# Optimization experiments

Hardware: AMD Instinct MI355X
Metric: run time of the kernel (lower is better)

The kernel has to match this reference:

```python
import jax, jax.numpy as jnp
import numpy as np

T, B, NIN = 256, 256, 512
NH, NEMB = 512, 256


def setup_inputs() -> dict:
    key = jax.random.key(0)
    ks = jax.random.split(key, 11)
    s = 0.02  # small init to keep tanh/sigmoid in active range
    return {
        "feats": jax.random.normal(ks[0], (T, B, NIN), jnp.float32),
        "h": jax.random.normal(ks[1], (B, NH), jnp.float32),
        "cur_embed": jax.random.normal(ks[2], (B, NEMB), jnp.float32),
        # i2h: Linear(nIn, nHidden, bias=False)
        "w_i2h": jax.random.normal(ks[3], (NH, NIN), jnp.float32) * s,
        # h2h: Linear(nHidden, nHidden) with bias
        "w_h2h": jax.random.normal(ks[4], (NH, NH), jnp.float32) * s,
        "b_h2h": jax.random.normal(ks[5], (NH,), jnp.float32) * s,
        # score: Linear(nHidden, 1, bias=False)
        "w_score": jax.random.normal(ks[6], (NH,), jnp.float32) * s,
        # GRUCell(nIn + num_embeddings, nHidden); gate order r, z, n
        "w_ih": jax.random.normal(ks[7], (3 * NH, NIN + NEMB), jnp.float32) * s,
        "w_hh": jax.random.normal(ks[8], (3 * NH, NH), jnp.float32) * s,
        "b_ih": jax.random.normal(ks[9], (3 * NH,), jnp.float32) * s,
        "b_hh": jax.random.normal(ks[10], (3 * NH,), jnp.float32) * s,
    }


def reference(feats, h, cur_embed, w_i2h, w_h2h, b_h2h, w_score,
              w_ih, w_hh, b_ih, b_hh):
    # MORAN branch, test=True (FractionalPickup is skipped at eval time).
    # feats: [T, B, nIn], h: [B, nHidden], cur_embed: [B, nEmb]
    feats_ = jnp.einsum('tbc,hc->tbh', feats, w_i2h)          # i2h, [T,B,H]
    h_ = h @ w_h2h.T + b_h2h                                   # h2h, [B,H]
    emit = jnp.einsum('tbh,h->tb', jnp.tanh(feats_ + h_[None]), w_score)
    alpha = jax.nn.softmax(emit, axis=0)                       # softmax over T
    context = jnp.einsum('tb,tbc->bc', alpha, feats)           # [B,nIn]
    x = jnp.concatenate([context, cur_embed], axis=1)          # [B,nIn+nEmb]
    # GRUCell
    gi = x @ w_ih.T + b_ih                                     # [B,3H]
    gh = h @ w_hh.T + b_hh                                     # [B,3H]
    gi_r, gi_z, gi_n = jnp.split(gi, 3, axis=1)
    gh_r, gh_z, gh_n = jnp.split(gh, 3, axis=1)
    r = jax.nn.sigmoid(gi_r + gh_r)
    z = jax.nn.sigmoid(gi_z + gh_z)
    n = jnp.tanh(gi_n + r * gh_n)
    nh = (1.0 - z) * n + z * h
    return nh, alpha
```

## Files before the change

### kernel.cpp

```cpp
#include <hip/hip_runtime.h>

typedef __bf16 bf16;
typedef __bf16 bf16x4 __attribute__((ext_vector_type(4)));
typedef __bf16 bf16x8 __attribute__((ext_vector_type(8)));
typedef float  f32x4  __attribute__((ext_vector_type(4)));

#define T_DIM 256
#define B_DIM 256
#define NIN   512
#define NH    512
#define NEMB  256
#define NX    768
#define NG    1536
#define MTOT  65536

__device__ __forceinline__ float fast_tanh(float x) {
    float e = __expf(2.0f * x);
    return 1.0f - 2.0f * __builtin_amdgcn_rcpf(e + 1.0f);
}
__device__ __forceinline__ float fast_sigmoid(float x) {
    return __builtin_amdgcn_rcpf(1.0f + __expf(-x));
}

__device__ __forceinline__ void gload_lds16(const bf16* g, bf16* l) {
    __builtin_amdgcn_global_load_lds(
        (const __attribute__((address_space(1))) void*)g,
        (__attribute__((address_space(3))) void*)l, 16, 0, 0);
}

__device__ __forceinline__ int csw(int row) { return (row >> 1) & 3; }

__global__ __launch_bounds__(256) void cvt_weights(
    const float* __restrict__ a0, const float* __restrict__ a1,
    const float* __restrict__ a2, const float* __restrict__ a3,
    const float* __restrict__ a4,
    bf16* __restrict__ b0, bf16* __restrict__ b1, bf16* __restrict__ b2,
    bf16* __restrict__ b3, bf16* __restrict__ b4) {
    const int N0 = 65536, N1 = 131072, N2 = 425984, N3 = 622592, N4 = 655360;
    for (int i = blockIdx.x * 256 + threadIdx.x; i < N4; i += gridDim.x * 256) {
        const float* s; bf16* d; int j;
        if (i < N0)      { s = a0; d = b0; j = i; }
        else if (i < N1) { s = a1; d = b1; j = i - N0; }
        else if (i < N2) { s = a2; d = b2; j = i - N1; }
        else if (i < N3) { s = a3; d = b3; j = i - N2; }
        else             { s = a4; d = b4; j = i - N3; }
        float4 v = reinterpret_cast<const float4*>(s)[j];
        bf16x4 o = { (bf16)v.x, (bf16)v.y, (bf16)v.z, (bf16)v.w };
        reinterpret_cast<bf16x4*>(d)[j] = o;
    }
}

__global__ __launch_bounds__(256) void gemm_bias(
    const bf16* __restrict__ A, const bf16* __restrict__ B,
    const float* __restrict__ bias, float* __restrict__ C,
    int M, int N, int K) {
    __shared__ bf16 At[64][40];
    __shared__ bf16 Bt[64][40];
    const int tid = threadIdx.x;
    const int m0 = blockIdx.y * 64, n0 = blockIdx.x * 64;
    const int wid = tid >> 6, lane = tid & 63, hi = lane >> 4, lo = lane & 15;
    const int srow = tid >> 2, sseg = tid & 3;
    f32x4 acc[4] = {};

    for (int kk = 0; kk < K; kk += 32) {
        bf16x8 av = *reinterpret_cast<const bf16x8*>(A + (size_t)(m0 + srow) * K + kk + sseg * 8);
        bf16x8 bv = *reinterpret_cast<const bf16x8*>(B + (size_t)(n0 + srow) * K + kk + sseg * 8);
        __syncthreads();
        *reinterpret_cast<bf16x8*>(&At[srow][sseg * 8]) = av;
        *reinterpret_cast<bf16x8*>(&Bt[srow][sseg * 8]) = bv;
        __syncthreads();
        bf16x8 a = *reinterpret_cast<const bf16x8*>(&At[wid * 16 + lo][hi * 8]);
#pragma unroll
        for (int nt = 0; nt < 4; ++nt) {
            bf16x8 b = *reinterpret_cast<const bf16x8*>(&Bt[nt * 16 + lo][hi * 8]);
            acc[nt] = __builtin_amdgcn_mfma_f32_16x16x32_bf16(a, b, acc[nt], 0, 0, 0);
        }
    }
#pragma unroll
    for (int nt = 0; nt < 4; ++nt) {
        int n = n0 + nt * 16 + lo;
        float bv = bias[n];
#pragma unroll
        for (int r = 0; r < 4; ++r) {
            int m = m0 + wid * 16 + hi * 4 + r;
            C[(size_t)m * N + n] = acc[nt][r] + bv;
        }
    }
}

__global__ __launch_bounds__(256, 3) void emit_kernel(
    const float* __restrict__ feats, const bf16* __restrict__ Wb,
    const float* __restrict__ hbuf, const float* __restrict__ wscore,
    float* __restrict__ emit_part) {
    __shared__ bf16 At[128 * 32];
    __shared__ bf16 Bt[128 * 32];
    __shared__ float ew[4][64];
    const int tid = threadIdx.x;
    const int tile = (blockIdx.x & 7) * 256 + (blockIdx.x >> 3);
    const int nb = tile & 3, mb = tile >> 2;
    const int m0 = mb * 128, n0g = nb * 128;
    const int wid = tid >> 6, lane = tid & 63, hi = lane >> 4, lo = lane & 15;
    const int wr = wid >> 1, wc = wid & 1;

    const int ar0 = tid >> 2, ac0 = tid & 3;
    const int ar1 = 64 + ar0, ac1 = ac0;
    const float* as0 = feats + (size_t)(m0 + ar0) * NIN + ac0 * 8;
    const float* as1 = feats + (size_t)(m0 + ar1) * NIN + ac1 * 8;
    bf16* aw0 = At + ar0 * 32 + ((ac0 ^ csw(ar0)) * 8);
    bf16* aw1 = At + ar1 * 32 + ((ac1 ^ csw(ar1)) * 8);
    const bf16* bs0 = Wb + (size_t)(n0g + ar0) * NIN + ((ac0 ^ csw(ar0)) * 8);
    const bf16* bs1 = Wb + (size_t)(n0g + ar1) * NIN + ((ac1 ^ csw(ar1)) * 8);
    bf16* bd0 = Bt + wid * 512;
    bf16* bd1 = Bt + 2048 + wid * 512;

    float4 f00 = *reinterpret_cast<const float4*>(as0);
    float4 f01 = *reinterpret_cast<const float4*>(as0 + 4);
    float4 f10 = *reinterpret_cast<const float4*>(as1);
    float4 f11 = *reinterpret_cast<const float4*>(as1 + 4);

    f32x4 acc[4][4] = {};
#pragma unroll
    for (int kk = 0; kk < 16; ++kk) {
        if (kk > 0) __syncthreads();
        bf16x8 o0 = { (bf16)f00.x, (bf16)f00.y, (bf16)f00.z, (bf16)f00.w,
                      (bf16)f01.x, (bf16)f01.y, (bf16)f01.z, (bf16)f01.w };
        bf16x8 o1 = { (bf16)f10.x, (bf16)f10.y, (bf16)f10.z, (bf16)f10.w,
                      (bf16)f11.x, (bf16)f11.y, (bf16)f11.z, (bf16)f11.w };
        *reinterpret_cast<bf16x8*>(aw0) = o0;
        *reinterpret_cast<bf16x8*>(aw1) = o1;
        gload_lds16(bs0 + kk * 32, bd0);
        gload_lds16(bs1 + kk * 32, bd1);
        __syncthreads();
        if (kk < 15) {
            f00 = *reinterpret_cast<const float4*>(as0 + (kk + 1) * 32);
            f01 = *reinterpret_cast<const float4*>(as0 + (kk + 1) * 32 + 4);
            f10 = *reinterpret_cast<const float4*>(as1 + (kk + 1) * 32);
            f11 = *reinterpret_cast<const float4*>(as1 + (kk + 1) * 32 + 4);
        }
        bf16x8 a[4], b[4];
#pragma unroll
        for (int st = 0; st < 4; ++st) {
            int row = wr * 64 + st * 16 + lo;
            a[st] = *reinterpret_cast<const bf16x8*>(
                At + row * 32 + ((hi ^ csw(row)) * 8));
        }
#pragma unroll
        for (int nt = 0; nt < 4; ++nt) {
            int col = wc * 64 + nt * 16 + lo;
            b[nt] = *reinterpret_cast<const bf16x8*>(
                Bt + col * 32 + ((hi ^ csw(col)) * 8));
        }
#pragma unroll
        for (int nt = 0; nt < 4; ++nt)
#pragma unroll
            for (int st = 0; st < 4; ++st)
                acc[nt][st] = __builtin_amdgcn_mfma_f32_16x16x32_bf16(
                    a[st], b[nt], acc[nt][st], 0, 0, 0);
    }

    float ep[4][4] = {};
    const int bbase = m0 & (B_DIM - 1);
#pragma unroll
    for (int nt = 0; nt < 4; ++nt) {
        int n = n0g + wc * 64 + nt * 16 + lo;
        float wsn = wscore[n];
#pragma unroll
        for (int st = 0; st < 4; ++st) {
#pragma unroll
            for (int r = 0; r < 4; ++r) {
                int b = bbase + wr * 64 + st * 16 + hi * 4 + r;
                float x = acc[nt][st][r] + hbuf[(size_t)b * NH + n];
                ep[st][r] += fast_tanh(x) * wsn;
            }
        }
    }
#pragma unroll
    for (int st = 0; st < 4; ++st)
#pragma unroll
        for (int r = 0; r < 4; ++r)
#pragma unroll
            for (int off = 1; off < 16; off <<= 1)
                ep[st][r] += __shfl_xor(ep[st][r], off, 64);

    if (lo == 0) {
#pragma unroll
        for (int st = 0; st < 4; ++st)
#pragma unroll
            for (int r = 0; r < 4; ++r)
                ew[wid][st * 16 + hi * 4 + r] = ep[st][r];
    }
    __syncthreads();
    if (tid < 128) {
        float s = ew[(tid >> 6) * 2][tid & 63] + ew[(tid >> 6) * 2 + 1][tid & 63];
        emit_part[(size_t)nb * MTOT + m0 + tid] = s;
    }
}

__global__ __launch_bounds__(256) void softmax_t(
    const float* __restrict__ emit_part, float* __restrict__ alpha,
    float* __restrict__ out_alpha) {
    int b = blockIdx.x, t = threadIdx.x;
    int wv = t >> 6, ln = t & 63;
    size_t m = (size_t)t * B_DIM + b;
    float e = emit_part[m] + emit_part[MTOT + m] +
              emit_part[2 * MTOT + m] + emit_part[3 * MTOT + m];
    float mx = e;
#pragma unroll
    for (int off = 32; off; off >>= 1) mx = fmaxf(mx, __shfl_xor(mx, off, 64));
    __shared__ float red[4], red2[4];
    if (ln == 0) red[wv] = mx;
    __syncthreads();
    mx = fmaxf(fmaxf(red[0], red[1]), fmaxf(red[2], red[3]));
    float p = __expf(e - mx);
    float s = p;
#pragma unroll
    for (int off = 32; off; off >>= 1) s += __shfl_xor(s, off, 64);
    if (ln == 0) red2[wv] = s;
    __syncthreads();
    float inv = __builtin_amdgcn_rcpf(red2[0] + red2[1] + red2[2] + red2[3]);
    float a = p * inv;
    alpha[m] = a;
    out_alpha[m] = a;
}

__global__ __launch_bounds__(256) void ctx_kernel(
    const float* __restrict__ feats, const float* __restrict__ alpha,
    const float* __restrict__ emb, bf16* __restrict__ x) {
    int b = blockIdx.x;
    __shared__ float al[T_DIM];
    __shared__ float red[4][512];
    int tid = threadIdx.x;
    al[tid] = alpha[(size_t)tid * B_DIM + b];
    __syncthreads();
    int c8 = tid & 63, tq = tid >> 6;
    float acc[8] = {};
#pragma unroll 4
    for (int t = tq * 64; t < tq * 64 + 64; ++t) {
        const float* src = feats + ((size_t)(t * B_DIM + b)) * NIN + c8 * 8;
        float4 v0 = *reinterpret_cast<const float4*>(src);
        float4 v1 = *reinterpret_cast<const float4*>(src + 4);
        float a = al[t];
        acc[0] += a * v0.x; acc[1] += a * v0.y; acc[2] += a * v0.z; acc[3] += a * v0.w;
        acc[4] += a * v1.x; acc[5] += a * v1.y; acc[6] += a * v1.z; acc[7] += a * v1.w;
    }
#pragma unroll
    for (int j = 0; j < 8; ++j) red[tq][c8 * 8 + j] = acc[j];
    __syncthreads();
#pragma unroll
    for (int k = 0; k < 2; ++k) {
        int c = tid * 2 + k;
        float s = red[0][c] + red[1][c] + red[2][c] + red[3][c];
        x[(size_t)b * NX + c] = (bf16)s;
    }
    x[(size_t)b * NX + NIN + tid] = (bf16)emb[(size_t)b * NEMB + tid];
}

__global__ __launch_bounds__(256) void gru_kernel(
    const float* __restrict__ gi, const float* __restrict__ gh,
    const float* __restrict__ h, float* __restrict__ out) {
    int idx = blockIdx.x * 256 + threadIdx.x;
    int b = idx >> 9, j = idx & 511;
    const float* gib = gi + (size_t)b * NG;
    const float* ghb = gh + (size_t)b * NG;
    float r = fast_sigmoid(gib[j] + ghb[j]);
    float z = fast_sigmoid(gib[NH + j] + ghb[NH + j]);
    float n = fast_tanh(gib[2 * NH + j] + r * ghb[2 * NH + j]);
    out[idx] = (1.0f - z) * n + z * h[idx];
}

extern "C" void kernel_launch(void* const* d_in, const int* in_sizes, int n_in,
                              void* d_out, int out_size, void* d_ws, size_t ws_size,
                              hipStream_t stream) {
    const float* feats = (const float*)d_in[0];
    const float* h     = (const float*)d_in[1];
    const float* emb   = (const float*)d_in[2];
    const float* w_i2h = (const float*)d_in[3];
    const float* w_h2h = (const float*)d_in[4];
    const float* b_h2h = (const float*)d_in[5];
    const float* w_sc  = (const float*)d_in[6];
    const float* w_ih  = (const float*)d_in[7];
    const float* w_hh  = (const float*)d_in[8];
    const float* b_ih  = (const float*)d_in[9];
    const float* b_hh  = (const float*)d_in[10];
    float* out = (float*)d_out;

    char* ws = (char*)d_ws;
    bf16*  w_i2h_b = (bf16*)(ws);
    bf16*  w_h2h_b = (bf16*)(ws + 524288);
    bf16*  w_ih_b  = (bf16*)(ws + 1048576);
    bf16*  w_hh_b  = (bf16*)(ws + 3407872);
    bf16*  h_b     = (bf16*)(ws + 4980736);
    bf16*  x_b     = (bf16*)(ws + 5242880);
    float* hbuf    = (float*)(ws + 5636096);
    float* emit_p  = (float*)(ws + 6160384);
    float* alpha   = (float*)(ws + 7208960);
    float* gi      = (float*)(ws + 7471104);
    float* gh      = (float*)(ws + 9043968);

    cvt_weights<<<1024, 256, 0, stream>>>(w_i2h, w_h2h, w_ih, w_hh, h,
                                          w_i2h_b, w_h2h_b, w_ih_b, w_hh_b, h_b);

    gemm_bias<<<dim3(8, 4), 256, 0, stream>>>(h_b, w_h2h_b, b_h2h, hbuf, 256, NH, NH);
    gemm_bias<<<dim3(24, 4), 256, 0, stream>>>(h_b, w_hh_b, b_hh, gh, 256, NG, NH);

    emit_kernel<<<2048, 256, 0, stream>>>(feats, w_i2h_b, hbuf, w_sc, emit_p);

    softmax_t<<<256, 256, 0, stream>>>(emit_p, alpha, out + 131072);

    ctx_kernel<<<256, 256, 0, stream>>>(feats, alpha, emb, x_b);

    gemm_bias<<<dim3(24, 4), 256, 0, stream>>>(x_b, w_ih_b, b_ih, gi, 256, NG, NX);

    gru_kernel<<<512, 256, 0, stream>>>(gi, gh, h, out);
}
```

Measured before the change: 127.5 us.

## Keep i2h weight fragments in registers and stream feats through double-buffered LDS

The emit kernel is restructured so each wave holds a 32-column slab of the i2h weight as pre-swizzled MFMA fragments in registers for the whole K=512. Each block then streams 512 rows of feats through a double-buffered LDS tile with 32x32x16 MFMAs. The weight conversion kernel now writes w_i2h in that fragment layout, and the grid splits N into two halves instead of four, so softmax sums only two partial emits. This removes the repeated per-tile weight LDS staging and halves the partial-emit traffic. In exchange it uses very high register pressure (32 bf16x8 fragments) and launches only 256 blocks of 512 threads, which may reduce occupancy and latency hiding.

```diff
diff --git a/kernel.cpp b/kernel.cpp
--- a/kernel.cpp
+++ b/kernel.cpp
@@ -4,6 +4,7 @@
 typedef __bf16 bf16x4 __attribute__((ext_vector_type(4)));
 typedef __bf16 bf16x8 __attribute__((ext_vector_type(8)));
 typedef float  f32x4  __attribute__((ext_vector_type(4)));
+typedef float  f32x16 __attribute__((ext_vector_type(16)));
 
 #define T_DIM 256
 #define B_DIM 256
@@ -22,14 +23,6 @@
     return __builtin_amdgcn_rcpf(1.0f + __expf(-x));
 }
 
-__device__ __forceinline__ void gload_lds16(const bf16* g, bf16* l) {
-    __builtin_amdgcn_global_load_lds(
-        (const __attribute__((address_space(1))) void*)g,
-        (__attribute__((address_space(3))) void*)l, 16, 0, 0);
-}
-
-__device__ __forceinline__ int csw(int row) { return (row >> 1) & 3; }
-
 __global__ __launch_bounds__(256) void cvt_weights(
     const float* __restrict__ a0, const float* __restrict__ a1,
     const float* __restrict__ a2, const float* __restrict__ a3,
@@ -38,15 +31,24 @@
     bf16* __restrict__ b3, bf16* __restrict__ b4) {
     const int N0 = 65536, N1 = 131072, N2 = 425984, N3 = 622592, N4 = 655360;
     for (int i = blockIdx.x * 256 + threadIdx.x; i < N4; i += gridDim.x * 256) {
-        const float* s; bf16* d; int j;
-        if (i < N0)      { s = a0; d = b0; j = i; }
+        const float* s; bf16* d; int j; bool img = false;
+        if (i < N0)      { s = a0; d = b0; j = i; img = true; }
         else if (i < N1) { s = a1; d = b1; j = i - N0; }
         else if (i < N2) { s = a2; d = b2; j = i - N1; }
         else if (i < N3) { s = a3; d = b3; j = i - N2; }
         else             { s = a4; d = b4; j = i - N3; }
         float4 v = reinterpret_cast<const float4*>(s)[j];
         bf16x4 o = { (bf16)v.x, (bf16)v.y, (bf16)v.z, (bf16)v.w };
-        reinterpret_cast<bf16x4*>(d)[j] = o;
+        if (img) {
+            int e = j * 4, col = e >> 9, K = e & 511;
+            int g = col >> 5, cl = col & 31;
+            int ks = K >> 4, kh = (K >> 3) & 1, j0 = K & 7;
+            int lane = kh * 32 + cl;
+            int off = (((g * 32 + ks) * 64) + lane) * 8 + j0;
+            *reinterpret_cast<bf16x4*>(d + off) = o;
+        } else {
+            reinterpret_cast<bf16x4*>(d)[j] = o;
+        }
     }
 }
 
@@ -88,111 +90,98 @@
     }
 }
 
-__global__ __launch_bounds__(256, 3) void emit_kernel(
-    const float* __restrict__ feats, const bf16* __restrict__ Wb,
+__global__ __launch_bounds__(512, 2) void emit_kernel(
+    const float* __restrict__ feats, const bf16* __restrict__ Wfrag,
     const float* __restrict__ hbuf, const float* __restrict__ wscore,
     float* __restrict__ emit_part) {
-    __shared__ bf16 At[128 * 32];
-    __shared__ bf16 Bt[128 * 32];
-    __shared__ float ew[4][64];
+    __shared__ bf16 Alds[2][32][516];
+    __shared__ float ew[2][8][32];
     const int tid = threadIdx.x;
-    const int tile = (blockIdx.x & 7) * 256 + (blockIdx.x >> 3);
-    const int nb = tile & 3, mb = tile >> 2;
-    const int m0 = mb * 128, n0g = nb * 128;
-    const int wid = tid >> 6, lane = tid & 63, hi = lane >> 4, lo = lane & 15;
-    const int wr = wid >> 1, wc = wid & 1;
-
-    const int ar0 = tid >> 2, ac0 = tid & 3;
-    const int ar1 = 64 + ar0, ac1 = ac0;
-    const float* as0 = feats + (size_t)(m0 + ar0) * NIN + ac0 * 8;
-    const float* as1 = feats + (size_t)(m0 + ar1) * NIN + ac1 * 8;
-    bf16* aw0 = At + ar0 * 32 + ((ac0 ^ csw(ar0)) * 8);
-    bf16* aw1 = At + ar1 * 32 + ((ac1 ^ csw(ar1)) * 8);
-    const bf16* bs0 = Wb + (size_t)(n0g + ar0) * NIN + ((ac0 ^ csw(ar0)) * 8);
-    const bf16* bs1 = Wb + (size_t)(n0g + ar1) * NIN + ((ac1 ^ csw(ar1)) * 8);
-    bf16* bd0 = Bt + wid * 512;
-    bf16* bd1 = Bt + 2048 + wid * 512;
-
-    float4 f00 = *reinterpret_cast<const float4*>(as0);
-    float4 f01 = *reinterpret_cast<const float4*>(as0 + 4);
-    float4 f10 = *reinterpret_cast<const float4*>(as1);
-    float4 f11 = *reinterpret_cast<const float4*>(as1 + 4);
-
-    f32x4 acc[4][4] = {};
-#pragma unroll
-    for (int kk = 0; kk < 16; ++kk) {
-        if (kk > 0) __syncthreads();
-        bf16x8 o0 = { (bf16)f00.x, (bf16)f00.y, (bf16)f00.z, (bf16)f00.w,
-                      (bf16)f01.x, (bf16)f01.y, (bf16)f01.z, (bf16)f01.w };
-        bf16x8 o1 = { (bf16)f10.x, (bf16)f10.y, (bf16)f10.z, (bf16)f10.w,
-                      (bf16)f11.x, (bf16)f11.y, (bf16)f11.z, (bf16)f11.w };
-        *reinterpret_cast<bf16x8*>(aw0) = o0;
-        *reinterpret_cast<bf16x8*>(aw1) = o1;
-        gload_lds16(bs0 + kk * 32, bd0);
-        gload_lds16(bs1 + kk * 32, bd1);
+    const int wid = tid >> 6, lane = tid & 63;
+    const int half = lane >> 5, l31 = lane & 31;
+    const int slab = blockIdx.x & 1, mb = blockIdx.x >> 1;
+    const int m0 = mb * 512;
+    const int col = slab * 256 + wid * 32 + l31;
+
+    const bf16* wsrc = Wfrag + (size_t)((slab * 8 + wid) * 32) * 512 + lane * 8;
+    bf16x8 bfr[32];
+#pragma unroll
+    for (int ks = 0; ks < 32; ++ks)
+        bfr[ks] = *reinterpret_cast<const bf16x8*>(wsrc + ks * 512);
+
+    const float* asrc = feats + (size_t)m0 * NIN + tid * 4;
+    const int awrow = tid >> 7, awcol = (tid & 127) * 4;
+
+    float4 st[8];
+#pragma unroll
+    for (int j = 0; j < 8; ++j)
+        st[j] = *reinterpret_cast<const float4*>(asrc + j * 2048);
+#pragma unroll
+    for (int j = 0; j < 8; ++j) {
+        bf16x4 o = { (bf16)st[j].x, (bf16)st[j].y, (bf16)st[j].z, (bf16)st[j].w };
+        *reinterpret_cast<bf16x4*>(&Alds[0][awrow + 4 * j][awcol]) = o;
+    }
+    __syncthreads();
+
+    const float wsl = wscore[col];
+
+    for (int it = 0; it < 16; ++it) {
+        const int cur = it & 1;
+        if (it < 15) {
+            const float* an = asrc + (size_t)(it + 1) * 32 * NIN;
+#pragma unroll
+            for (int j = 0; j < 8; ++j)
+                st[j] = *reinterpret_cast<const float4*>(an + j * 2048);
+        }
+
+        f32x16 acc0 = {}, acc1 = {};
+#pragma unroll
+        for (int ks = 0; ks < 32; ks += 2) {
+            const bf16* ap0 = &Alds[cur][l31][ks * 16 + half * 8];
+            bf16x4 p0 = *reinterpret_cast<const bf16x4*>(ap0);
+            bf16x4 p1 = *reinterpret_cast<const bf16x4*>(ap0 + 4);
+            bf16x8 a0 = { p0[0], p0[1], p0[2], p0[3], p1[0], p1[1], p1[2], p1[3] };
+            acc0 = __builtin_amdgcn_mfma_f32_32x32x16_bf16(a0, bfr[ks], acc0, 0, 0, 0);
+            const bf16* ap1 = &Alds[cur][l31][(ks + 1) * 16 + half * 8];
+            bf16x4 q0 = *reinterpret_cast<const bf16x4*>(ap1);
+            bf16x4 q1 = *reinterpret_cast<const bf16x4*>(ap1 + 4);
+            bf16x8 a1 = { q0[0], q0[1], q0[2], q0[3], q1[0], q1[1], q1[2], q1[3] };
+            acc1 = __builtin_amdgcn_mfma_f32_32x32x16_bf16(a1, bfr[ks + 1], acc1, 0, 0, 0);
+        }
+
+        float e[16];
+#pragma unroll
+        for (int r = 0; r < 16; ++r) {
+            int row = (r & 3) + 8 * (r >> 2) + 4 * half;
+            int brow = (it * 32 + row) & (B_DIM - 1);
+            float x = acc0[r] + acc1[r] + hbuf[(size_t)brow * NH + col];
+            e[r] = fast_tanh(x) * wsl;
+        }
+#pragma unroll
+        for (int r = 0; r < 16; ++r)
+#pragma unroll
+            for (int off = 1; off < 32; off <<= 1)
+                e[r] += __shfl_xor(e[r], off, 64);
+        if (l31 == 0) {
+#pragma unroll
+            for (int r = 0; r < 16; ++r)
+                ew[cur][wid][(r & 3) + 8 * (r >> 2) + 4 * half] = e[r];
+        }
+
+        if (it < 15) {
+#pragma unroll
+            for (int j = 0; j < 8; ++j) {
+                bf16x4 o = { (bf16)st[j].x, (bf16)st[j].y, (bf16)st[j].z, (bf16)st[j].w };
+                *reinterpret_cast<bf16x4*>(&Alds[cur ^ 1][awrow + 4 * j][awcol]) = o;
+            }
+        }
         __syncthreads();
-        if (kk < 15) {
-            f00 = *reinterpret_cast<const float4*>(as0 + (kk + 1) * 32);
-            f01 = *reinterpret_cast<const float4*>(as0 + (kk + 1) * 32 + 4);
-            f10 = *reinterpret_cast<const float4*>(as1 + (kk + 1) * 32);
-            f11 = *reinterpret_cast<const float4*>(as1 + (kk + 1) * 32 + 4);
-        }
-        bf16x8 a[4], b[4];
-#pragma unroll
-        for (int st = 0; st < 4; ++st) {
-            int row = wr * 64 + st * 16 + lo;
-            a[st] = *reinterpret_cast<const bf16x8*>(
-                At + row * 32 + ((hi ^ csw(row)) * 8));
-        }
-#pragma unroll
-        for (int nt = 0; nt < 4; ++nt) {
-            int col = wc * 64 + nt * 16 + lo;
-            b[nt] = *reinterpret_cast<const bf16x8*>(
-                Bt + col * 32 + ((hi ^ csw(col)) * 8));
-        }
-#pragma unroll
-        for (int nt = 0; nt < 4; ++nt)
-#pragma unroll
-            for (int st = 0; st < 4; ++st)
-                acc[nt][st] = __builtin_amdgcn_mfma_f32_16x16x32_bf16(
-                    a[st], b[nt], acc[nt][st], 0, 0, 0);
-    }
-
-    float ep[4][4] = {};
-    const int bbase = m0 & (B_DIM - 1);
-#pragma unroll
-    for (int nt = 0; nt < 4; ++nt) {
-        int n = n0g + wc * 64 + nt * 16 + lo;
-        float wsn = wscore[n];
-#pragma unroll
-        for (int st = 0; st < 4; ++st) {
-#pragma unroll
-            for (int r = 0; r < 4; ++r) {
-                int b = bbase + wr * 64 + st * 16 + hi * 4 + r;
-                float x = acc[nt][st][r] + hbuf[(size_t)b * NH + n];
-                ep[st][r] += fast_tanh(x) * wsn;
-            }
-        }
-    }
-#pragma unroll
-    for (int st = 0; st < 4; ++st)
-#pragma unroll
-        for (int r = 0; r < 4; ++r)
-#pragma unroll
-            for (int off = 1; off < 16; off <<= 1)
-                ep[st][r] += __shfl_xor(ep[st][r], off, 64);
-
-    if (lo == 0) {
-#pragma unroll
-        for (int st = 0; st < 4; ++st)
-#pragma unroll
-            for (int r = 0; r < 4; ++r)
-                ew[wid][st * 16 + hi * 4 + r] = ep[st][r];
-    }
-    __syncthreads();
-    if (tid < 128) {
-        float s = ew[(tid >> 6) * 2][tid & 63] + ew[(tid >> 6) * 2 + 1][tid & 63];
-        emit_part[(size_t)nb * MTOT + m0 + tid] = s;
+        if (tid < 32) {
+            float s = 0.0f;
+#pragma unroll
+            for (int w = 0; w < 8; ++w) s += ew[cur][w][tid];
+            emit_part[(size_t)slab * MTOT + m0 + it * 32 + tid] = s;
+        }
     }
 }
 
@@ -202,8 +191,7 @@
     int b = blockIdx.x, t = threadIdx.x;
     int wv = t >> 6, ln = t & 63;
     size_t m = (size_t)t * B_DIM + b;
-    float e = emit_part[m] + emit_part[MTOT + m] +
-              emit_part[2 * MTOT + m] + emit_part[3 * MTOT + m];
+    float e = emit_part[m] + emit_part[MTOT + m];
     float mx = e;
 #pragma unroll
     for (int off = 32; off; off >>= 1) mx = fmaxf(mx, __shfl_xor(mx, off, 64));
@@ -285,7 +273,7 @@
     float* out = (float*)d_out;
 
     char* ws = (char*)d_ws;
-    bf16*  w_i2h_b = (bf16*)(ws);
+    bf16*  Wfrag   = (bf16*)(ws);
     bf16*  w_h2h_b = (bf16*)(ws + 524288);
     bf16*  w_ih_b  = (bf16*)(ws + 1048576);
     bf16*  w_hh_b  = (bf16*)(ws + 3407872);
@@ -293,17 +281,17 @@
     bf16*  x_b     = (bf16*)(ws + 5242880);
     float* hbuf    = (float*)(ws + 5636096);
     float* emit_p  = (float*)(ws + 6160384);
-    float* alpha   = (float*)(ws + 7208960);
-    float* gi      = (float*)(ws + 7471104);
-    float* gh      = (float*)(ws + 9043968);
+    float* alpha   = (float*)(ws + 6684672);
+    float* gi      = (float*)(ws + 6946816);
+    float* gh      = (float*)(ws + 8519680);
 
     cvt_weights<<<1024, 256, 0, stream>>>(w_i2h, w_h2h, w_ih, w_hh, h,
-                                          w_i2h_b, w_h2h_b, w_ih_b, w_hh_b, h_b);
+                                          Wfrag, w_h2h_b, w_ih_b, w_hh_b, h_b);
 
     gemm_bias<<<dim3(8, 4), 256, 0, stream>>>(h_b, w_h2h_b, b_h2h, hbuf, 256, NH, NH);
     gemm_bias<<<dim3(24, 4), 256, 0, stream>>>(h_b, w_hh_b, b_hh, gh, 256, NG, NH);
 
-    emit_kernel<<<2048, 256, 0, stream>>>(feats, w_i2h_b, hbuf, w_sc, emit_p);
+    emit_kernel<<<256, 512, 0, stream>>>(feats, Wfrag, hbuf, w_sc, emit_p);
 
     softmax_t<<<256, 256, 0, stream>>>(emit_p, alpha, out + 131072);
 
```

After: 137.5 us. 7.9% more time.
